# Kernel tuning notes

Measured on AMD Instinct MI355X. Metric: run time of the kernel, lower is better.

## Reference

```python
import jax, jax.numpy as jnp
import numpy as np
from jax import lax

B, T, E, H, N_LAYERS = 64, 256, 512, 512, 2


def _lstm_stack(x, params):
    # x: [B, T, in] -> returns full top-layer hidden sequence [T, B, H]
    xs = jnp.swapaxes(x, 0, 1)  # time-major [T, B, in]
    for (Wih, Whh, bih, bhh) in params:
        def step(carry, xt, Wih=Wih, Whh=Whh, bih=bih, bhh=bhh):
            h, c = carry
            gates = xt @ Wih.T + bih + h @ Whh.T + bhh  # [B, 4H]
            i, f, g, o = jnp.split(gates, 4, axis=-1)   # PyTorch gate order i,f,g,o
            i = jax.nn.sigmoid(i)
            f = jax.nn.sigmoid(f)
            g = jnp.tanh(g)
            o = jax.nn.sigmoid(o)
            c = f * c + i * g
            h = o * jnp.tanh(c)
            return (h, c), h
        nb = xs.shape[1]
        hdim = Whh.shape[1]
        init = (jnp.zeros((nb, hdim), xs.dtype), jnp.zeros((nb, hdim), xs.dtype))
        _, xs = lax.scan(step, init, xs)
    return xs  # [T, B, H]


def setup_inputs() -> dict:
    key = jax.random.key(0)
    ks = jax.random.split(key, 16)
    s = 0.04  # ~1/sqrt(H) init scale
    inp = {"text": jax.random.normal(ks[0], (B, T, E), dtype=jnp.float32)}
    # layer 0: input dim E; layer 1: input dim H
    inp["W_ih0"] = jax.random.normal(ks[1], (4 * H, E), dtype=jnp.float32) * s
    inp["W_hh0"] = jax.random.normal(ks[2], (4 * H, H), dtype=jnp.float32) * s
    inp["b_ih0"] = jax.random.normal(ks[3], (4 * H,), dtype=jnp.float32) * s
    inp["b_hh0"] = jax.random.normal(ks[4], (4 * H,), dtype=jnp.float32) * s
    inp["W_ih1"] = jax.random.normal(ks[5], (4 * H, H), dtype=jnp.float32) * s
    inp["W_hh1"] = jax.random.normal(ks[6], (4 * H, H), dtype=jnp.float32) * s
    inp["b_ih1"] = jax.random.normal(ks[7], (4 * H,), dtype=jnp.float32) * s
    inp["b_hh1"] = jax.random.normal(ks[8], (4 * H,), dtype=jnp.float32) * s
    inp["W_lin"] = jax.random.normal(ks[9], (1, 2 * H), dtype=jnp.float32) * s
    inp["b_lin"] = jax.random.normal(ks[10], (1,), dtype=jnp.float32) * s
    return inp


def reference(text, W_ih0, W_hh0, b_ih0, b_hh0, W_ih1, W_hh1, b_ih1, b_hh1, W_lin, b_lin):
    params = [(W_ih0, W_hh0, b_ih0, b_hh0), (W_ih1, W_hh1, b_ih1, b_hh1)]
    out_f = _lstm_stack(text, params)[-1]                       # [B, H] last step, fwd pass
    out_r = _lstm_stack(jnp.flip(text, axis=1), params)[-1]     # [B, H] last step, reversed input (same weights, as in source)
    out = jnp.concatenate([out_f, out_r], axis=1)               # [B, 2H]
    # dropout is identity in eval mode
    return out @ W_lin.T + b_lin                                # [B, 1]
```

## Files before the change

### kernel.cpp

```cpp
#include <hip/hip_runtime.h>
#include <stdint.h>

constexpr int HD   = 512;
constexpr int TS   = 256;
constexpr int NB   = 64;
constexpr int MBR  = 128;
constexpr int SLAB = MBR * HD;
constexpr int NG   = 8;
constexpr int NS   = 16;

typedef __attribute__((ext_vector_type(8))) short bf16x8;
typedef __attribute__((ext_vector_type(4))) float f32x4;

__device__ __forceinline__ unsigned short f2bf(float f){
  union { float f; unsigned u; } v; v.f = f;
  unsigned r = v.u + 0x7fffu + ((v.u >> 16) & 1u);
  return (unsigned short)(r >> 16);
}
__device__ __forceinline__ float fsig(float x){ return 1.f / (1.f + __expf(-x)); }
__device__ __forceinline__ float ftanh(float x){ return 1.f - 2.f / (__expf(2.f * x) + 1.f); }
__device__ __forceinline__ void vdrain(){ asm volatile("s_waitcnt vmcnt(0)" ::: "memory"); }

__device__ __forceinline__ int ld_flag_sc1(const int* p){
  int v;
  asm volatile("global_load_dword %0, %1, off sc0 sc1\n\ts_waitcnt vmcnt(0)"
               : "=v"(v) : "v"(p) : "memory");
  return v;
}
__device__ __forceinline__ void st_sc1_b32(void* p, int v){
  asm volatile("global_store_dword %0, %1, off sc0 sc1" :: "v"(p), "v"(v) : "memory");
}

__device__ __forceinline__ void ld16_sc1(const void* p, f32x4* r){
  asm volatile(
    "global_load_dwordx4 %0,  %16, off sc0 sc1\n\t"
    "global_load_dwordx4 %1,  %16, off offset:64 sc0 sc1\n\t"
    "global_load_dwordx4 %2,  %16, off offset:128 sc0 sc1\n\t"
    "global_load_dwordx4 %3,  %16, off offset:192 sc0 sc1\n\t"
    "global_load_dwordx4 %4,  %16, off offset:256 sc0 sc1\n\t"
    "global_load_dwordx4 %5,  %16, off offset:320 sc0 sc1\n\t"
    "global_load_dwordx4 %6,  %16, off offset:384 sc0 sc1\n\t"
    "global_load_dwordx4 %7,  %16, off offset:448 sc0 sc1\n\t"
    "global_load_dwordx4 %8,  %16, off offset:512 sc0 sc1\n\t"
    "global_load_dwordx4 %9,  %16, off offset:576 sc0 sc1\n\t"
    "global_load_dwordx4 %10, %16, off offset:640 sc0 sc1\n\t"
    "global_load_dwordx4 %11, %16, off offset:704 sc0 sc1\n\t"
    "global_load_dwordx4 %12, %16, off offset:768 sc0 sc1\n\t"
    "global_load_dwordx4 %13, %16, off offset:832 sc0 sc1\n\t"
    "global_load_dwordx4 %14, %16, off offset:896 sc0 sc1\n\t"
    "global_load_dwordx4 %15, %16, off offset:960 sc0 sc1\n\t"
    "s_waitcnt vmcnt(0)"
    : "=&v"(r[0]), "=&v"(r[1]), "=&v"(r[2]), "=&v"(r[3]),
      "=&v"(r[4]), "=&v"(r[5]), "=&v"(r[6]), "=&v"(r[7]),
      "=&v"(r[8]), "=&v"(r[9]), "=&v"(r[10]), "=&v"(r[11]),
      "=&v"(r[12]), "=&v"(r[13]), "=&v"(r[14]), "=&v"(r[15])
    : "v"(p) : "memory");
}
__device__ __forceinline__ bf16x8 pack8(float4 a, float4 b){
  bf16x8 w;
  w[0]=(short)f2bf(a.x); w[1]=(short)f2bf(a.y); w[2]=(short)f2bf(a.z); w[3]=(short)f2bf(a.w);
  w[4]=(short)f2bf(b.x); w[5]=(short)f2bf(b.y); w[6]=(short)f2bf(b.z); w[7]=(short)f2bf(b.w);
  return w;
}

__global__ __launch_bounds__(512, 1)
void lstm_persist(const float* __restrict__ text,
                  const float* __restrict__ Wih0, const float* __restrict__ Whh0,
                  const float* __restrict__ bih0, const float* __restrict__ bhh0,
                  const float* __restrict__ Wih1, const float* __restrict__ Whh1,
                  const float* __restrict__ bih1, const float* __restrict__ bhh1,
                  unsigned short* __restrict__ h0x,
                  unsigned short* __restrict__ h1r,
                  float* __restrict__ H1f,
                  int* __restrict__ F)
{
  extern __shared__ unsigned short Blds[];
  __shared__ int s_abort;

  const int wg    = blockIdx.x;
  const int layer = wg >> 7;
  const int grp   = (wg >> 4) & 7;
  const int slice = wg & 15;
  const int m0    = grp * 16;
  const int u0    = slice * 32;
  const int tid   = threadIdx.x;
  const int wv    = tid >> 6;
  const int l     = tid & 63;
  const int lj    = l & 15;
  const int lk    = l >> 4;

  if (tid == 0) s_abort = 0;

  int* F0g = F + ((0 * NG + grp) * TS) * NS;
  int* F1g = F + ((1 * NG + grp) * TS) * NS;

  const float* Wihl = layer ? Wih1 : Wih0;
  const float* Whhl = layer ? Whh1 : Whh0;

  for (int it = tid; it < 128 * 64; it += 512){
    int c = it >> 6, kg = it & 63;
    int unit = u0 + (c >> 2);
    int gate = c & 3;
    const float* s = Wihl + (size_t)(gate * HD + unit) * HD + kg * 8;
    *(bf16x8*)((char*)Blds + c * 1024 + ((kg ^ (c & 7)) << 4)) =
        pack8(((const float4*)s)[0], ((const float4*)s)[1]);
  }

  const int j      = wv * 16 + lj;
  const int myunit = u0 + (j >> 2);
  const int mygate = j & 3;
  bf16x8 bPost[16];
  {
    const float* s0 = Whhl + (size_t)(mygate * HD + myunit) * HD + lk * 8;
    #pragma unroll
    for (int kk = 0; kk < 16; ++kk){
      const float* s = s0 + kk * 32;
      bPost[kk] = pack8(((const float4*)s)[0], ((const float4*)s)[1]);
    }
  }
  const float bgv = (layer ? bih1 : bih0)[mygate * HD + myunit]
                  + (layer ? bhh1 : bhh0)[mygate * HD + myunit];
  const int aoff  = (m0 + lj) * HD + lk * 8;
  const int cboff = j * 1024;
  const int swz   = lj & 7;

  float cst[4] = {0.f, 0.f, 0.f, 0.f};
  __syncthreads();

  auto ldsB = [&](int kg)->bf16x8 {
    return *(const bf16x8*)((const char*)Blds + cboff + ((kg ^ swz) << 4));
  };
  auto pollwait = [&](const int* base){
    if (*(volatile int*)&s_abort) return;
    const int* fp = base + (l & 15);
    int it = 0;
    for (;;){
      int v = ld_flag_sc1(fp);
      if (__all(v != 0)) break;
      ++it;
      if (it > 4096){
        if (it > 2000000){ s_abort = 1; break; }
        __builtin_amdgcn_s_sleep(1);
      }
    }
  };
  auto postHalf = [&](const f32x4* raw, f32x4& acc){
    #pragma unroll
    for (int kk = 0; kk < 16; ++kk)
      acc = __builtin_amdgcn_mfma_f32_16x16x32_bf16(
              __builtin_bit_cast(bf16x8, raw[kk]), bPost[kk], acc, 0, 0, 0);
  };
  auto cellstore = [&](const f32x4& aP, const f32x4& aQ,
                       unsigned short* __restrict__ hslab, bool wrF){
    #pragma unroll
    for (int r = 0; r < 4; ++r){
      float v  = aP[r] + aQ[r] + bgv;
      float v1 = __shfl_xor(v, 1);
      float v2 = __shfl_xor(v, 2);
      float v3 = __shfl_xor(v, 3);
      auto pick = [&](int m)->float {
        return m == 0 ? v : (m == 1 ? v1 : (m == 2 ? v2 : v3));
      };
      float gi = pick(mygate);
      float gf = pick(mygate ^ 1);
      float gg = pick(mygate ^ 2);
      float go = pick(mygate ^ 3);
      float i_ = fsig(gi);
      float f_ = fsig(gf);
      float g_ = ftanh(gg);
      float o_ = fsig(go);
      float c  = f_ * cst[r] + i_ * g_;
      cst[r] = c;
      float h  = o_ * ftanh(c);
      int row  = m0 + lk * 4 + r;
      int hb   = (int)f2bf(h);
      int pb   = __shfl_xor(hb, 4);
      if ((j & 7) == 0)
        st_sc1_b32((char*)hslab + ((size_t)row * HD + myunit) * 2,
                   (hb & 0xffff) | (pb << 16));
      if (wrF && mygate == 0)
        H1f[(size_t)row * HD + myunit] = h;
    }
  };
  auto preX = [&](int t, f32x4& acc){
    int arow = m0 + lj;
    int b    = arow & 63;
    int ts2  = (arow < 64) ? t : (TS - 1 - t);
    const float* src = text + ((size_t)b * TS + ts2) * HD + lk * 8;
    acc = (f32x4){0.f, 0.f, 0.f, 0.f};
    #pragma unroll
    for (int kk = 0; kk < 16; ++kk){
      const float* s = src + kk * 32;
      bf16x8 a = pack8(((const float4*)s)[0], ((const float4*)s)[1]);
      acc = __builtin_amdgcn_mfma_f32_16x16x32_bf16(a, ldsB(kk * 4 + lk), acc, 0, 0, 0);
    }
  };

  if (layer == 0){
    f32x4 accPre;
    preX(0, accPre);
    for (int t = 0; t < TS; ++t){
      f32x4 accPost = {0.f, 0.f, 0.f, 0.f};
      if (t > 0){
        if (wv == 0) pollwait(F0g + (t - 1) * NS);
        __syncthreads();
        f32x4 raw[16];
        ld16_sc1(h0x + (size_t)(t - 1) * SLAB + aoff, raw);
        postHalf(raw, accPost);
      }
      cellstore(accPre, accPost, h0x + (size_t)t * SLAB, false);
      vdrain();
      __syncthreads();
      if (tid == 0) st_sc1_b32(F0g + t * NS + slice, 1);
      if (t + 1 < TS) preX(t + 1, accPre);
    }
  } else {
    for (int t = 0; t < TS; ++t){
      if (wv == 0) pollwait(F0g + t * NS);
      __syncthreads();
      f32x4 accPre = {0.f, 0.f, 0.f, 0.f};
      {
        f32x4 rawI[16];
        ld16_sc1(h0x + (size_t)t * SLAB + aoff, rawI);
        #pragma unroll
        for (int kk = 0; kk < 16; ++kk)
          accPre = __builtin_amdgcn_mfma_f32_16x16x32_bf16(
                     __builtin_bit_cast(bf16x8, rawI[kk]), ldsB(kk * 4 + lk),
                     accPre, 0, 0, 0);
      }
      f32x4 accPost = {0.f, 0.f, 0.f, 0.f};
      if (t > 0){
        if (wv == 0) pollwait(F1g + (t - 1) * NS);
        __syncthreads();
        f32x4 rawR[16];
        ld16_sc1(h1r + (size_t)((t - 1) & 3) * SLAB + aoff, rawR);
        postHalf(rawR, accPost);
      }
      cellstore(accPre, accPost, h1r + (size_t)(t & 3) * SLAB, t == TS - 1);
      vdrain();
      __syncthreads();
      if (tid == 0) st_sc1_b32(F1g + t * NS + slice, 1);
    }
  }
}

__global__ void final_linear(const float* __restrict__ H1f, const float* __restrict__ Wlin,
                             const float* __restrict__ blin, float* __restrict__ out){
  int b = blockIdx.x, l = threadIdx.x;
  float s = 0.f;
  for (int jj = l; jj < HD; jj += 64) s += H1f[(size_t)b * HD + jj]        * Wlin[jj];
  for (int jj = l; jj < HD; jj += 64) s += H1f[(size_t)(NB + b) * HD + jj] * Wlin[HD + jj];
  #pragma unroll
  for (int off = 32; off; off >>= 1) s += __shfl_down(s, off);
  if (l == 0) out[b] = s + blin[0];
}

extern "C" void kernel_launch(void* const* d_in, const int* in_sizes, int n_in,
                              void* d_out, int out_size, void* d_ws, size_t ws_size,
                              hipStream_t stream)
{
  const float* text = (const float*)d_in[0];
  const float* Wih0 = (const float*)d_in[1];
  const float* Whh0 = (const float*)d_in[2];
  const float* bih0 = (const float*)d_in[3];
  const float* bhh0 = (const float*)d_in[4];
  const float* Wih1 = (const float*)d_in[5];
  const float* Whh1 = (const float*)d_in[6];
  const float* bih1 = (const float*)d_in[7];
  const float* bhh1 = (const float*)d_in[8];
  const float* Wlin = (const float*)d_in[9];
  const float* blin = (const float*)d_in[10];

  uint8_t* p = (uint8_t*)d_ws;
  unsigned short* h0x = (unsigned short*)p; p += (size_t)TS * SLAB * 2;
  unsigned short* h1r = (unsigned short*)p; p += (size_t)4 * SLAB * 2;
  float* H1f          = (float*)p;          p += (size_t)SLAB * 4;
  int* F              = (int*)p;            p += (size_t)2 * NG * TS * NS * 4;

  hipMemsetAsync(F, 0, (size_t)2 * NG * TS * NS * 4, stream);

  hipFuncSetAttribute((const void*)lstm_persist,
                      hipFuncAttributeMaxDynamicSharedMemorySize, 131072);

  const float* A0 = text;
  const float *A1 = Wih0, *A2 = Whh0, *A3 = bih0, *A4 = bhh0;
  const float *A5 = Wih1, *A6 = Whh1, *A7 = bih1, *A8 = bhh1;
  unsigned short* B0 = h0x; unsigned short* B1 = h1r;
  float* B2 = H1f; int* B3 = F;
  void* args[] = {(void*)&A0,
                  (void*)&A1, (void*)&A2, (void*)&A3, (void*)&A4,
                  (void*)&A5, (void*)&A6, (void*)&A7, (void*)&A8,
                  (void*)&B0, (void*)&B1, (void*)&B2, (void*)&B3};
  hipLaunchCooperativeKernel((void*)lstm_persist, dim3(256), dim3(512),
                             args, 131072, stream);

  final_linear<<<NB, 64, 0, stream>>>(H1f, Wlin, blin, (float*)d_out);
}
```

Baseline: 3.493 ms.

## Stage recurrent hidden tile into LDS once per block instead of per-wave loads

Replaces per-wave 16-load global fetches of the previous hidden state with a cooperative block-wide copy into a swizzled LDS tile, read by all waves for the MFMA. Layer 1's input projection for the next step is moved after the flag publish so the dependency chain on the recurrent flag is shorter. This reduces redundant global/L2 traffic per step at the cost of extra barriers and 16KB more LDS.

```diff
diff --git a/kernel.cpp b/kernel.cpp
--- a/kernel.cpp
+++ b/kernel.cpp
@@ -29,32 +29,6 @@
 }
 __device__ __forceinline__ void st_sc1_b32(void* p, int v){
   asm volatile("global_store_dword %0, %1, off sc0 sc1" :: "v"(p), "v"(v) : "memory");
-}
-
-__device__ __forceinline__ void ld16_sc1(const void* p, f32x4* r){
-  asm volatile(
-    "global_load_dwordx4 %0,  %16, off sc0 sc1\n\t"
-    "global_load_dwordx4 %1,  %16, off offset:64 sc0 sc1\n\t"
-    "global_load_dwordx4 %2,  %16, off offset:128 sc0 sc1\n\t"
-    "global_load_dwordx4 %3,  %16, off offset:192 sc0 sc1\n\t"
-    "global_load_dwordx4 %4,  %16, off offset:256 sc0 sc1\n\t"
-    "global_load_dwordx4 %5,  %16, off offset:320 sc0 sc1\n\t"
-    "global_load_dwordx4 %6,  %16, off offset:384 sc0 sc1\n\t"
-    "global_load_dwordx4 %7,  %16, off offset:448 sc0 sc1\n\t"
-    "global_load_dwordx4 %8,  %16, off offset:512 sc0 sc1\n\t"
-    "global_load_dwordx4 %9,  %16, off offset:576 sc0 sc1\n\t"
-    "global_load_dwordx4 %10, %16, off offset:640 sc0 sc1\n\t"
-    "global_load_dwordx4 %11, %16, off offset:704 sc0 sc1\n\t"
-    "global_load_dwordx4 %12, %16, off offset:768 sc0 sc1\n\t"
-    "global_load_dwordx4 %13, %16, off offset:832 sc0 sc1\n\t"
-    "global_load_dwordx4 %14, %16, off offset:896 sc0 sc1\n\t"
-    "global_load_dwordx4 %15, %16, off offset:960 sc0 sc1\n\t"
-    "s_waitcnt vmcnt(0)"
-    : "=&v"(r[0]), "=&v"(r[1]), "=&v"(r[2]), "=&v"(r[3]),
-      "=&v"(r[4]), "=&v"(r[5]), "=&v"(r[6]), "=&v"(r[7]),
-      "=&v"(r[8]), "=&v"(r[9]), "=&v"(r[10]), "=&v"(r[11]),
-      "=&v"(r[12]), "=&v"(r[13]), "=&v"(r[14]), "=&v"(r[15])
-    : "v"(p) : "memory");
 }
 __device__ __forceinline__ bf16x8 pack8(float4 a, float4 b){
   bf16x8 w;
@@ -74,7 +48,9 @@
                   float* __restrict__ H1f,
                   int* __restrict__ F)
 {
-  extern __shared__ unsigned short Blds[];
+  extern __shared__ char lds[];
+  char* Wlds  = lds;
+  char* Htile = lds + 131072;
   __shared__ int s_abort;
 
   const int wg    = blockIdx.x;
@@ -102,7 +78,7 @@
     int unit = u0 + (c >> 2);
     int gate = c & 3;
     const float* s = Wihl + (size_t)(gate * HD + unit) * HD + kg * 8;
-    *(bf16x8*)((char*)Blds + c * 1024 + ((kg ^ (c & 7)) << 4)) =
+    *(bf16x8*)(Wlds + c * 1024 + ((kg ^ (c & 7)) << 4)) =
         pack8(((const float4*)s)[0], ((const float4*)s)[1]);
   }
 
@@ -120,7 +96,6 @@
   }
   const float bgv = (layer ? bih1 : bih0)[mygate * HD + myunit]
                   + (layer ? bhh1 : bhh0)[mygate * HD + myunit];
-  const int aoff  = (m0 + lj) * HD + lk * 8;
   const int cboff = j * 1024;
   const int swz   = lj & 7;
 
@@ -128,7 +103,23 @@
   __syncthreads();
 
   auto ldsB = [&](int kg)->bf16x8 {
-    return *(const bf16x8*)((const char*)Blds + cboff + ((kg ^ swz) << 4));
+    return *(const bf16x8*)(Wlds + cboff + ((kg ^ swz) << 4));
+  };
+  auto ldsH = [&](int kc)->bf16x8 {
+    int byte = kc * 64 + lk * 16;
+    return *(const bf16x8*)(Htile + lj * 1024 + (byte ^ ((lj & 15) << 4)));
+  };
+  auto stage = [&](const unsigned short* src){
+    const int r = tid >> 5, c = tid & 31;
+    const char* gp = (const char*)(src + (size_t)(m0 + r) * HD) + c * 32;
+    f32x4 t0, t1;
+    asm volatile("global_load_dwordx4 %0, %2, off sc0 sc1\n\t"
+                 "global_load_dwordx4 %1, %2, off offset:16 sc0 sc1\n\t"
+                 "s_waitcnt vmcnt(0)"
+                 : "=&v"(t0), "=&v"(t1) : "v"(gp) : "memory");
+    char* rb = Htile + r * 1024;
+    *(f32x4*)(rb + (((c * 32)      ^ ((r & 15) << 4)))) = t0;
+    *(f32x4*)(rb + (((c * 32 + 16) ^ ((r & 15) << 4)))) = t1;
   };
   auto pollwait = [&](const int* base){
     if (*(volatile int*)&s_abort) return;
@@ -143,12 +134,6 @@
         __builtin_amdgcn_s_sleep(1);
       }
     }
-  };
-  auto postHalf = [&](const f32x4* raw, f32x4& acc){
-    #pragma unroll
-    for (int kk = 0; kk < 16; ++kk)
-      acc = __builtin_amdgcn_mfma_f32_16x16x32_bf16(
-              __builtin_bit_cast(bf16x8, raw[kk]), bPost[kk], acc, 0, 0, 0);
   };
   auto cellstore = [&](const f32x4& aP, const f32x4& aQ,
                        unsigned short* __restrict__ hslab, bool wrF){
@@ -204,9 +189,12 @@
       if (t > 0){
         if (wv == 0) pollwait(F0g + (t - 1) * NS);
         __syncthreads();
-        f32x4 raw[16];
-        ld16_sc1(h0x + (size_t)(t - 1) * SLAB + aoff, raw);
-        postHalf(raw, accPost);
+        stage(h0x + (size_t)(t - 1) * SLAB);
+        __syncthreads();
+        #pragma unroll
+        for (int kk = 0; kk < 16; ++kk)
+          accPost = __builtin_amdgcn_mfma_f32_16x16x32_bf16(
+                      ldsH(kk), bPost[kk], accPost, 0, 0, 0);
       }
       cellstore(accPre, accPost, h0x + (size_t)t * SLAB, false);
       vdrain();
@@ -215,31 +203,44 @@
       if (t + 1 < TS) preX(t + 1, accPre);
     }
   } else {
+    f32x4 accPre = {0.f, 0.f, 0.f, 0.f};
+    {
+      if (wv == 0) pollwait(F0g + 0);
+      __syncthreads();
+      stage(h0x);
+      __syncthreads();
+      #pragma unroll
+      for (int kk = 0; kk < 16; ++kk)
+        accPre = __builtin_amdgcn_mfma_f32_16x16x32_bf16(
+                   ldsH(kk), ldsB(kk * 4 + lk), accPre, 0, 0, 0);
+    }
     for (int t = 0; t < TS; ++t){
-      if (wv == 0) pollwait(F0g + t * NS);
-      __syncthreads();
-      f32x4 accPre = {0.f, 0.f, 0.f, 0.f};
-      {
-        f32x4 rawI[16];
-        ld16_sc1(h0x + (size_t)t * SLAB + aoff, rawI);
+      f32x4 accPost = {0.f, 0.f, 0.f, 0.f};
+      if (t > 0){
+        if (wv == 0) pollwait(F1g + (t - 1) * NS);
+        __syncthreads();
+        stage(h1r + (size_t)((t - 1) & 3) * SLAB);
+        __syncthreads();
+        #pragma unroll
+        for (int kk = 0; kk < 16; ++kk)
+          accPost = __builtin_amdgcn_mfma_f32_16x16x32_bf16(
+                      ldsH(kk), bPost[kk], accPost, 0, 0, 0);
+      }
+      cellstore(accPre, accPost, h1r + (size_t)(t & 3) * SLAB, t == TS - 1);
+      vdrain();
+      __syncthreads();
+      if (tid == 0) st_sc1_b32(F1g + t * NS + slice, 1);
+      if (t + 1 < TS){
+        if (wv == 0) pollwait(F0g + (t + 1) * NS);
+        __syncthreads();
+        stage(h0x + (size_t)(t + 1) * SLAB);
+        __syncthreads();
+        accPre = (f32x4){0.f, 0.f, 0.f, 0.f};
         #pragma unroll
         for (int kk = 0; kk < 16; ++kk)
           accPre = __builtin_amdgcn_mfma_f32_16x16x32_bf16(
-                     __builtin_bit_cast(bf16x8, rawI[kk]), ldsB(kk * 4 + lk),
-                     accPre, 0, 0, 0);
-      }
-      f32x4 accPost = {0.f, 0.f, 0.f, 0.f};
-      if (t > 0){
-        if (wv == 0) pollwait(F1g + (t - 1) * NS);
-        __syncthreads();
-        f32x4 rawR[16];
-        ld16_sc1(h1r + (size_t)((t - 1) & 3) * SLAB + aoff, rawR);
-        postHalf(rawR, accPost);
-      }
-      cellstore(accPre, accPost, h1r + (size_t)(t & 3) * SLAB, t == TS - 1);
-      vdrain();
-      __syncthreads();
-      if (tid == 0) st_sc1_b32(F1g + t * NS + slice, 1);
+                     ldsH(kk), ldsB(kk * 4 + lk), accPre, 0, 0, 0);
+      }
     }
   }
 }
@@ -280,7 +281,7 @@
   hipMemsetAsync(F, 0, (size_t)2 * NG * TS * NS * 4, stream);
 
   hipFuncSetAttribute((const void*)lstm_persist,
-                      hipFuncAttributeMaxDynamicSharedMemorySize, 131072);
+                      hipFuncAttributeMaxDynamicSharedMemorySize, 147456);
 
   const float* A0 = text;
   const float *A1 = Wih0, *A2 = Whh0, *A3 = bih0, *A4 = bhh0;
@@ -292,7 +293,7 @@
                   (void*)&A5, (void*)&A6, (void*)&A7, (void*)&A8,
                   (void*)&B0, (void*)&B1, (void*)&B2, (void*)&B3};
   hipLaunchCooperativeKernel((void*)lstm_persist, dim3(256), dim3(512),
-                             args, 131072, stream);
+                             args, 147456, stream);
 
   final_linear<<<NB, 64, 0, stream>>>(H1f, Wlin, blin, (float*)d_out);
 }
```

After: 3.857 ms. +10.4%, slower.
